# Kernel optimization log

Measured on AMD Instinct MI355X. Metric: run time of the kernel, lower is better.

The kernel has to match this reference:

```python
import jax, jax.numpy as jnp
import numpy as np

QMIN, QMAX = -128.0, 127.0


def setup_inputs() -> dict:
    key = jax.random.key(0)
    kx, kw, kb = jax.random.split(key, 3)
    B, S, K, M = 4, 2048, 4096, 4096
    x = jax.random.normal(kx, (B, S, K), dtype=jnp.float32)
    bound = 1.0 / np.sqrt(K)  # kaiming_uniform(a=sqrt(5)) -> U(-1/sqrt(fan_in), 1/sqrt(fan_in))
    W = jax.random.uniform(kw, (M, K), dtype=jnp.float32, minval=-bound, maxval=bound)
    b = jax.random.uniform(kb, (M,), dtype=jnp.float32, minval=-bound, maxval=bound)
    return {"x": x, "W": W, "b": b}


def _quant_weights_rowwise(W):
    # symmetric per-row int8: scale = absmax/127
    absmax = jnp.max(jnp.abs(W), axis=1, keepdims=True)  # [M,1]
    scale = jnp.where(absmax > 0, absmax / QMAX, 1.0)
    Wq = jnp.clip(jnp.round(W / scale), QMIN, QMAX)
    return Wq, scale


def _quant_acts_per_token(X):
    # asymmetric per-token (per column of X.t()) int8 with zero-point
    xmin = jnp.min(X, axis=1, keepdims=True)  # [N,1]
    xmax = jnp.max(X, axis=1, keepdims=True)
    rng = xmax - xmin
    scale = jnp.where(rng > 0, rng / (QMAX - QMIN), 1.0)
    zp = jnp.clip(jnp.round(QMIN - xmin / scale), QMIN, QMAX)
    Xq = jnp.clip(jnp.round(X / scale + zp), QMIN, QMAX)
    return Xq, scale, zp


def reference(x, W, b):
    B, S, K = x.shape
    X = x.reshape(-1, K)  # [N, K]
    Wq, row_scale = _quant_weights_rowwise(W)          # [M,K], [M,1]
    Xq, col_scale, zp = _quant_acts_per_token(X)       # [N,K], [N,1], [N,1]
    # fused dequant-GEMM: Y = ((Xq - zp) * col_scale) @ (Wq * row_scale).T
    Wdq = Wq * row_scale                               # [M,K]
    Xdq = (Xq - zp) * col_scale                        # [N,K]
    Y = jnp.einsum('nk,mk->nm', Xdq, Wdq) + b          # [N,M]
    return Y.reshape(B, S, -1)
```

## Files before the change

kernel.cpp:

```cpp
#include <hip/hip_runtime.h>
#include <stdint.h>


typedef __attribute__((ext_vector_type(4)))  int int4v;
typedef __attribute__((ext_vector_type(16))) int int16v;

__device__ __forceinline__ void async_load16(const void* g, void* l) {
    __builtin_amdgcn_global_load_lds(
        (const __attribute__((address_space(1))) void*)g,
        (__attribute__((address_space(3))) void*)l, 16, 0, 0);
}

__device__ __forceinline__ int quant_clip(float v) {
    return (int)fminf(fmaxf(rintf(v), -128.f), 127.f);
}

__global__ __launch_bounds__(256) void quant_kernel(
    const float* __restrict__ W, const float* __restrict__ X,
    int8_t* __restrict__ Wq, int8_t* __restrict__ Xq,
    float* __restrict__ row_scale, int* __restrict__ wsum,
    float* __restrict__ col_scale, int* __restrict__ zp, int M, int K) {
    const int blk  = blockIdx.x;
    const int tid  = threadIdx.x;
    const int lane = tid & 63;
    const int wv   = tid >> 6;
    __shared__ float sred0[4], sred1[4];
    __shared__ int   isum[4];

    if (blk < M) {
        const int row = blk;
        const float4* w4 = (const float4*)(W + (size_t)row * K);
        float4 vals[4];
        float amax = 0.f;
#pragma unroll
        for (int i = 0; i < 4; ++i) {
            float4 v = w4[tid + i * 256];
            vals[i] = v;
            amax = fmaxf(amax, fmaxf(fmaxf(fabsf(v.x), fabsf(v.y)),
                                     fmaxf(fabsf(v.z), fabsf(v.w))));
        }
#pragma unroll
        for (int off = 32; off > 0; off >>= 1)
            amax = fmaxf(amax, __shfl_down(amax, off, 64));
        if (lane == 0) sred0[wv] = amax;
        __syncthreads();
        amax = fmaxf(fmaxf(sred0[0], sred0[1]), fmaxf(sred0[2], sred0[3]));

        const float scale = (amax > 0.f) ? (amax / 127.f) : 1.f;
        const float inv   = 1.f / scale;

        int ssum = 0;
        int* wq32 = (int*)(Wq + (size_t)row * K);
#pragma unroll
        for (int i = 0; i < 4; ++i) {
            float4 v = vals[i];
            int q0 = quant_clip(v.x * inv);
            int q1 = quant_clip(v.y * inv);
            int q2 = quant_clip(v.z * inv);
            int q3 = quant_clip(v.w * inv);
            ssum += q0 + q1 + q2 + q3;
            wq32[tid + i * 256] =
                (q0 & 0xff) | ((q1 & 0xff) << 8) | ((q2 & 0xff) << 16) | ((q3 & 0xff) << 24);
        }
#pragma unroll
        for (int off = 32; off > 0; off >>= 1)
            ssum += __shfl_down(ssum, off, 64);
        if (lane == 0) isum[wv] = ssum;
        __syncthreads();
        if (tid == 0) {
            wsum[row] = isum[0] + isum[1] + isum[2] + isum[3];
            row_scale[row] = scale;
        }
    } else {
        const int row = blk - M;
        const float4* x4 = (const float4*)(X + (size_t)row * K);
        float4 vals[4];
        float vmin = 3.402823466e+38f, vmax = -3.402823466e+38f;
#pragma unroll
        for (int i = 0; i < 4; ++i) {
            float4 v = x4[tid + i * 256];
            vals[i] = v;
            vmin = fminf(vmin, fminf(fminf(v.x, v.y), fminf(v.z, v.w)));
            vmax = fmaxf(vmax, fmaxf(fmaxf(v.x, v.y), fmaxf(v.z, v.w)));
        }
#pragma unroll
        for (int off = 32; off > 0; off >>= 1) {
            vmin = fminf(vmin, __shfl_down(vmin, off, 64));
            vmax = fmaxf(vmax, __shfl_down(vmax, off, 64));
        }
        if (lane == 0) { sred0[wv] = vmin; sred1[wv] = vmax; }
        __syncthreads();
        vmin = fminf(fminf(sred0[0], sred0[1]), fminf(sred0[2], sred0[3]));
        vmax = fmaxf(fmaxf(sred1[0], sred1[1]), fmaxf(sred1[2], sred1[3]));

        const float rng   = vmax - vmin;
        const float scale = (rng > 0.f) ? (rng / 255.f) : 1.f;
        const float inv   = 1.f / scale;
        const float zpf   = fminf(fmaxf(rintf(-128.f - vmin * inv), -128.f), 127.f);

        int* xq32 = (int*)(Xq + (size_t)row * K);
#pragma unroll
        for (int i = 0; i < 4; ++i) {
            float4 v = vals[i];
            int q0 = quant_clip(v.x * inv + zpf);
            int q1 = quant_clip(v.y * inv + zpf);
            int q2 = quant_clip(v.z * inv + zpf);
            int q3 = quant_clip(v.w * inv + zpf);
            xq32[tid + i * 256] =
                (q0 & 0xff) | ((q1 & 0xff) << 8) | ((q2 & 0xff) << 16) | ((q3 & 0xff) << 24);
        }
        if (tid == 0) {
            col_scale[row] = scale;
            zp[row] = (int)zpf;
        }
    }
}

__global__ __launch_bounds__(256) void gemm_i8_kernel(
    const int8_t* __restrict__ Xq, const int8_t* __restrict__ Wq,
    const float* __restrict__ cs, const int* __restrict__ zp,
    const float* __restrict__ rs, const int* __restrict__ wsum,
    const float* __restrict__ bias, float* __restrict__ out,
    int N, int M, int K) {
    __shared__ __align__(16) int8_t As[128 * 64];
    __shared__ __align__(16) int8_t Bs[128 * 64];

    const int t    = threadIdx.x;
    const int wv   = t >> 6;
    const int lane = t & 63;
    const int r32  = lane & 31;
    const int half = lane >> 5;

    const int m0 = blockIdx.x * 128;
    const int n0 = blockIdx.y * 128;
    const int wn = (wv >> 1) * 64;
    const int wm = (wv & 1) * 64;

    int16v acc[2][2];
#pragma unroll
    for (int i = 0; i < 2; ++i)
#pragma unroll
        for (int j = 0; j < 2; ++j)
            acc[i][j] = (int16v)(0);

    const int r0 = t >> 2;
    const int c0 = (t & 3) ^ ((r0 >> 1) & 3);
    const size_t gA0 = (size_t)(n0 + r0) * K + c0 * 16;
    const size_t gA1 = (size_t)(n0 + 64 + r0) * K + c0 * 16;
    const size_t gB0 = (size_t)(m0 + r0) * K + c0 * 16;
    const size_t gB1 = (size_t)(m0 + 64 + r0) * K + c0 * 16;
    int8_t* lA0 = As + wv * 1024;
    int8_t* lA1 = As + 4096 + wv * 1024;
    int8_t* lB0 = Bs + wv * 1024;
    int8_t* lB1 = Bs + 4096 + wv * 1024;

    int abase[2], bbase[2], asw[2], bsw[2];
#pragma unroll
    for (int i = 0; i < 2; ++i) {
        const int ra = wn + i * 32 + r32;
        abase[i] = ra * 64;
        asw[i]   = (ra >> 1) & 3;
        const int rb = wm + i * 32 + r32;
        bbase[i] = rb * 64;
        bsw[i]   = (rb >> 1) & 3;
    }

    for (int k0 = 0; k0 < K; k0 += 64) {
        async_load16(Xq + gA0 + k0, lA0);
        async_load16(Xq + gA1 + k0, lA1);
        async_load16(Wq + gB0 + k0, lB0);
        async_load16(Wq + gB1 + k0, lB1);
        __syncthreads();

        int4v a[2][2], b[2][2];
#pragma unroll
        for (int s = 0; s < 2; ++s) {
            const int ch = s * 2 + half;
#pragma unroll
            for (int i = 0; i < 2; ++i) {
                a[s][i] = *(const int4v*)(As + abase[i] + ((ch ^ asw[i]) << 4));
                b[s][i] = *(const int4v*)(Bs + bbase[i] + ((ch ^ bsw[i]) << 4));
            }
        }
#pragma unroll
        for (int s = 0; s < 2; ++s)
#pragma unroll
            for (int i = 0; i < 2; ++i)
#pragma unroll
                for (int j = 0; j < 2; ++j)
                    acc[i][j] = __builtin_amdgcn_mfma_i32_32x32x32_i8(
                        a[s][i], b[s][j], acc[i][j], 0, 0, 0);
        __syncthreads();
    }

    int   mm[2];
    float rsv[2], bv[2];
    int   wsv[2];
#pragma unroll
    for (int j = 0; j < 2; ++j) {
        mm[j]  = m0 + wm + j * 32 + r32;
        rsv[j] = rs[mm[j]];
        bv[j]  = bias[mm[j]];
        wsv[j] = wsum[mm[j]];
    }
#pragma unroll
    for (int i = 0; i < 2; ++i) {
        const int nb = n0 + wn + i * 32 + half * 4;
#pragma unroll
        for (int reg = 0; reg < 16; ++reg) {
            const int n = nb + (reg & 3) + 8 * (reg >> 2);
            const float csn = cs[n];
            const int   zpn = zp[n];
#pragma unroll
            for (int j = 0; j < 2; ++j) {
                const int ival = acc[i][j][reg] - zpn * wsv[j];
                out[(size_t)n * M + mm[j]] = csn * rsv[j] * (float)ival + bv[j];
            }
        }
    }
}

extern "C" void kernel_launch(void* const* d_in, const int* in_sizes, int n_in,
                              void* d_out, int out_size, void* d_ws, size_t ws_size,
                              hipStream_t stream) {
    const float* x = (const float*)d_in[0];
    const float* W = (const float*)d_in[1];
    const float* b = (const float*)d_in[2];
    float* out = (float*)d_out;

    const int M = in_sizes[2];
    const int K = in_sizes[1] / M;
    const int N = in_sizes[0] / K;

    int8_t* Xq = (int8_t*)d_ws;
    int8_t* Wq = Xq + (size_t)N * K;
    float* cs  = (float*)(Wq + (size_t)M * K);
    int* zps   = (int*)(cs + N);
    float* rs  = (float*)(zps + N);
    int* wsum  = (int*)(rs + M);

    quant_kernel<<<dim3(M + N), dim3(256), 0, stream>>>(
        W, x, Wq, Xq, rs, wsum, cs, zps, M, K);
    gemm_i8_kernel<<<dim3(M / 128, N / 128), dim3(256), 0, stream>>>(
        Xq, Wq, cs, zps, rs, wsum, b, out, N, M, K);
}
```

Measured before the change: 445.0 us.

## Use 256x256 int8 GEMM tiles with double-buffered async LDS pipeline

```diff
diff --git a/kernel.cpp b/kernel.cpp
--- a/kernel.cpp
+++ b/kernel.cpp
@@ -116,81 +116,122 @@
     }
 }
 
-__global__ __launch_bounds__(256) void gemm_i8_kernel(
+#define REGION(buf, mat, kh) (lds + ((((buf) * 2 + (mat)) * 2 + (kh)) << 14))
+
+__device__ __forceinline__ void compute_half(
+    const int8_t* Ar, const int8_t* Br,
+    const int aoff[4], const int boff[2],
+    const int half, const int sw4, int16v (&acc)[4][2]) {
+    __builtin_amdgcn_s_setprio(1);
+#pragma unroll
+    for (int ss = 0; ss < 2; ++ss) {
+        const int cc = ((((ss << 1) + half) ^ sw4) << 4);
+        int4v a[4], b[2];
+#pragma unroll
+        for (int i = 0; i < 4; ++i)
+            a[i] = *(const int4v*)(Ar + aoff[i] + cc);
+#pragma unroll
+        for (int j = 0; j < 2; ++j)
+            b[j] = *(const int4v*)(Br + boff[j] + cc);
+#pragma unroll
+        for (int i = 0; i < 4; ++i)
+#pragma unroll
+            for (int j = 0; j < 2; ++j)
+                acc[i][j] = __builtin_amdgcn_mfma_i32_32x32x32_i8(
+                    a[i], b[j], acc[i][j], 0, 0, 0);
+    }
+    __builtin_amdgcn_s_setprio(0);
+}
+
+__global__ __launch_bounds__(512, 2) void gemm_i8_kernel(
     const int8_t* __restrict__ Xq, const int8_t* __restrict__ Wq,
     const float* __restrict__ cs, const int* __restrict__ zp,
     const float* __restrict__ rs, const int* __restrict__ wsum,
     const float* __restrict__ bias, float* __restrict__ out,
     int N, int M, int K) {
-    __shared__ __align__(16) int8_t As[128 * 64];
-    __shared__ __align__(16) int8_t Bs[128 * 64];
+    __shared__ __align__(16) int8_t lds[131072];
 
     const int t    = threadIdx.x;
     const int wv   = t >> 6;
     const int lane = t & 63;
     const int r32  = lane & 31;
     const int half = lane >> 5;
-
-    const int m0 = blockIdx.x * 128;
-    const int n0 = blockIdx.y * 128;
-    const int wn = (wv >> 1) * 64;
-    const int wm = (wv & 1) * 64;
-
-    int16v acc[2][2];
-#pragma unroll
-    for (int i = 0; i < 2; ++i)
+    const int wn   = wv >> 2;
+    const int wm   = wv & 3;
+
+    const int nMB = M >> 8;
+    const int per = ((M >> 8) * (N >> 8)) >> 3;
+    const int lin = blockIdx.x;
+    const int g   = (lin & 7) * per + (lin >> 3);
+    const int m0  = (g % nMB) << 8;
+    const int n0  = (g / nMB) << 8;
+
+    const int NT = K >> 7;
+
+    const int lrow   = (wv << 4) + (lane >> 2);
+    const int srcOff = (((lane & 3) ^ ((lane >> 3) & 3)) << 4);
+    const int8_t* gA0 = Xq + (size_t)(n0 + lrow) * K + srcOff;
+    const int8_t* gA1 = Xq + (size_t)(n0 + 128 + lrow) * K + srcOff;
+    const int8_t* gB0 = Wq + (size_t)(m0 + lrow) * K + srcOff;
+    const int8_t* gB1 = Wq + (size_t)(m0 + 128 + lrow) * K + srcOff;
+    const int wvOff = wv << 10;
+
+    int aoff[4], boff[2];
+#pragma unroll
+    for (int i = 0; i < 4; ++i) aoff[i] = (((wn << 7) + i * 32 + r32) << 6);
+#pragma unroll
+    for (int j = 0; j < 2; ++j) boff[j] = (((wm << 6) + j * 32 + r32) << 6);
+    const int sw4 = (r32 >> 1) & 3;
+
+    int16v acc[4][2];
+#pragma unroll
+    for (int i = 0; i < 4; ++i)
 #pragma unroll
         for (int j = 0; j < 2; ++j)
             acc[i][j] = (int16v)(0);
 
-    const int r0 = t >> 2;
-    const int c0 = (t & 3) ^ ((r0 >> 1) & 3);
-    const size_t gA0 = (size_t)(n0 + r0) * K + c0 * 16;
-    const size_t gA1 = (size_t)(n0 + 64 + r0) * K + c0 * 16;
-    const size_t gB0 = (size_t)(m0 + r0) * K + c0 * 16;
-    const size_t gB1 = (size_t)(m0 + 64 + r0) * K + c0 * 16;
-    int8_t* lA0 = As + wv * 1024;
-    int8_t* lA1 = As + 4096 + wv * 1024;
-    int8_t* lB0 = Bs + wv * 1024;
-    int8_t* lB1 = Bs + 4096 + wv * 1024;
-
-    int abase[2], bbase[2], asw[2], bsw[2];
-#pragma unroll
-    for (int i = 0; i < 2; ++i) {
-        const int ra = wn + i * 32 + r32;
-        abase[i] = ra * 64;
-        asw[i]   = (ra >> 1) & 3;
-        const int rb = wm + i * 32 + r32;
-        bbase[i] = rb * 64;
-        bsw[i]   = (rb >> 1) & 3;
-    }
-
-    for (int k0 = 0; k0 < K; k0 += 64) {
-        async_load16(Xq + gA0 + k0, lA0);
-        async_load16(Xq + gA1 + k0, lA1);
-        async_load16(Wq + gB0 + k0, lB0);
-        async_load16(Wq + gB1 + k0, lB1);
-        __syncthreads();
-
-        int4v a[2][2], b[2][2];
-#pragma unroll
-        for (int s = 0; s < 2; ++s) {
-            const int ch = s * 2 + half;
-#pragma unroll
-            for (int i = 0; i < 2; ++i) {
-                a[s][i] = *(const int4v*)(As + abase[i] + ((ch ^ asw[i]) << 4));
-                b[s][i] = *(const int4v*)(Bs + bbase[i] + ((ch ^ bsw[i]) << 4));
-            }
-        }
-#pragma unroll
-        for (int s = 0; s < 2; ++s)
-#pragma unroll
-            for (int i = 0; i < 2; ++i)
-#pragma unroll
-                for (int j = 0; j < 2; ++j)
-                    acc[i][j] = __builtin_amdgcn_mfma_i32_32x32x32_i8(
-                        a[s][i], b[s][j], acc[i][j], 0, 0, 0);
-        __syncthreads();
+    {
+        int8_t* r;
+        r = REGION(0, 0, 0) + wvOff; async_load16(gA0, r);       async_load16(gA1, r + 8192);
+        r = REGION(0, 1, 0) + wvOff; async_load16(gB0, r);       async_load16(gB1, r + 8192);
+        r = REGION(0, 0, 1) + wvOff; async_load16(gA0 + 64, r);  async_load16(gA1 + 64, r + 8192);
+        r = REGION(0, 1, 1) + wvOff; async_load16(gB0 + 64, r);  async_load16(gB1 + 64, r + 8192);
+        r = REGION(1, 0, 0) + wvOff; async_load16(gA0 + 128, r); async_load16(gA1 + 128, r + 8192);
+        r = REGION(1, 1, 0) + wvOff; async_load16(gB0 + 128, r); async_load16(gB1 + 128, r + 8192);
+    }
+    asm volatile("s_waitcnt vmcnt(8)" ::: "memory");
+    __builtin_amdgcn_s_barrier();
+
+    for (int tt = 0; tt < NT; ++tt) {
+        const int buf = tt & 1;
+        {
+            const int tn = (tt + 1 < NT) ? tt + 1 : NT - 1;
+            const int ko = (tn << 7) + 64;
+            int8_t* r;
+            r = REGION(buf ^ 1, 0, 1) + wvOff;
+            async_load16(gA0 + ko, r); async_load16(gA1 + ko, r + 8192);
+            r = REGION(buf ^ 1, 1, 1) + wvOff;
+            async_load16(gB0 + ko, r); async_load16(gB1 + ko, r + 8192);
+
+            compute_half(REGION(buf, 0, 0), REGION(buf, 1, 0), aoff, boff, half, sw4, acc);
+
+            asm volatile("s_waitcnt vmcnt(8)" ::: "memory");
+            __builtin_amdgcn_s_barrier();
+        }
+        {
+            const int tn = (tt + 2 < NT) ? tt + 2 : NT - 1;
+            const int ko = (tn << 7);
+            int8_t* r;
+            r = REGION(buf, 0, 0) + wvOff;
+            async_load16(gA0 + ko, r); async_load16(gA1 + ko, r + 8192);
+            r = REGION(buf, 1, 0) + wvOff;
+            async_load16(gB0 + ko, r); async_load16(gB1 + ko, r + 8192);
+
+            compute_half(REGION(buf, 0, 1), REGION(buf, 1, 1), aoff, boff, half, sw4, acc);
+
+            asm volatile("s_waitcnt vmcnt(8)" ::: "memory");
+            __builtin_amdgcn_s_barrier();
+        }
     }
 
     int   mm[2];
@@ -198,17 +239,17 @@
     int   wsv[2];
 #pragma unroll
     for (int j = 0; j < 2; ++j) {
-        mm[j]  = m0 + wm + j * 32 + r32;
+        mm[j]  = m0 + (wm << 6) + j * 32 + r32;
         rsv[j] = rs[mm[j]];
         bv[j]  = bias[mm[j]];
         wsv[j] = wsum[mm[j]];
     }
 #pragma unroll
-    for (int i = 0; i < 2; ++i) {
-        const int nb = n0 + wn + i * 32 + half * 4;
+    for (int i = 0; i < 4; ++i) {
+        const int nbase = n0 + (wn << 7) + i * 32 + (half << 2);
 #pragma unroll
         for (int reg = 0; reg < 16; ++reg) {
-            const int n = nb + (reg & 3) + 8 * (reg >> 2);
+            const int n = nbase + (reg & 3) + 8 * (reg >> 2);
             const float csn = cs[n];
             const int   zpn = zp[n];
 #pragma unroll
@@ -241,6 +282,6 @@
 
     quant_kernel<<<dim3(M + N), dim3(256), 0, stream>>>(
         W, x, Wq, Xq, rs, wsum, cs, zps, M, K);
-    gemm_i8_kernel<<<dim3(M / 128, N / 128), dim3(256), 0, stream>>>(
+    gemm_i8_kernel<<<dim3((M >> 8) * (N >> 8)), dim3(512), 0, stream>>>(
         Xq, Wq, cs, zps, rs, wsum, b, out, N, M, K);
 }
```

New measurement: 409.9 us. 7.9% less time.

## Triple-buffer int8 GEMM LDS loads with XCD-aware block swizzle

Applied to the files above, without the earlier changes.

```diff
diff --git a/kernel.cpp b/kernel.cpp
--- a/kernel.cpp
+++ b/kernel.cpp
@@ -116,81 +116,101 @@
     }
 }
 
-__global__ __launch_bounds__(256) void gemm_i8_kernel(
+__global__ __launch_bounds__(256, 4) void gemm_i8_kernel(
     const int8_t* __restrict__ Xq, const int8_t* __restrict__ Wq,
     const float* __restrict__ cs, const int* __restrict__ zp,
     const float* __restrict__ rs, const int* __restrict__ wsum,
     const float* __restrict__ bias, float* __restrict__ out,
     int N, int M, int K) {
-    __shared__ __align__(16) int8_t As[128 * 64];
-    __shared__ __align__(16) int8_t Bs[128 * 64];
+    __shared__ __align__(16) int8_t lds[49152];
 
     const int t    = threadIdx.x;
     const int wv   = t >> 6;
     const int lane = t & 63;
     const int r32  = lane & 31;
     const int half = lane >> 5;
-
-    const int m0 = blockIdx.x * 128;
-    const int n0 = blockIdx.y * 128;
-    const int wn = (wv >> 1) * 64;
-    const int wm = (wv & 1) * 64;
-
-    int16v acc[2][2];
-#pragma unroll
-    for (int i = 0; i < 2; ++i)
-#pragma unroll
-        for (int j = 0; j < 2; ++j)
-            acc[i][j] = (int16v)(0);
-
-    const int r0 = t >> 2;
-    const int c0 = (t & 3) ^ ((r0 >> 1) & 3);
-    const size_t gA0 = (size_t)(n0 + r0) * K + c0 * 16;
-    const size_t gA1 = (size_t)(n0 + 64 + r0) * K + c0 * 16;
-    const size_t gB0 = (size_t)(m0 + r0) * K + c0 * 16;
-    const size_t gB1 = (size_t)(m0 + 64 + r0) * K + c0 * 16;
-    int8_t* lA0 = As + wv * 1024;
-    int8_t* lA1 = As + 4096 + wv * 1024;
-    int8_t* lB0 = Bs + wv * 1024;
-    int8_t* lB1 = Bs + 4096 + wv * 1024;
-
-    int abase[2], bbase[2], asw[2], bsw[2];
-#pragma unroll
-    for (int i = 0; i < 2; ++i) {
-        const int ra = wn + i * 32 + r32;
-        abase[i] = ra * 64;
-        asw[i]   = (ra >> 1) & 3;
-        const int rb = wm + i * 32 + r32;
-        bbase[i] = rb * 64;
-        bsw[i]   = (rb >> 1) & 3;
-    }
-
-    for (int k0 = 0; k0 < K; k0 += 64) {
-        async_load16(Xq + gA0 + k0, lA0);
-        async_load16(Xq + gA1 + k0, lA1);
-        async_load16(Wq + gB0 + k0, lB0);
-        async_load16(Wq + gB1 + k0, lB1);
-        __syncthreads();
-
-        int4v a[2][2], b[2][2];
-#pragma unroll
-        for (int s = 0; s < 2; ++s) {
-            const int ch = s * 2 + half;
-#pragma unroll
-            for (int i = 0; i < 2; ++i) {
-                a[s][i] = *(const int4v*)(As + abase[i] + ((ch ^ asw[i]) << 4));
-                b[s][i] = *(const int4v*)(Bs + bbase[i] + ((ch ^ bsw[i]) << 4));
-            }
-        }
-#pragma unroll
-        for (int s = 0; s < 2; ++s)
-#pragma unroll
-            for (int i = 0; i < 2; ++i)
-#pragma unroll
-                for (int j = 0; j < 2; ++j)
-                    acc[i][j] = __builtin_amdgcn_mfma_i32_32x32x32_i8(
-                        a[s][i], b[s][j], acc[i][j], 0, 0, 0);
-        __syncthreads();
+    const int wn   = wv >> 1;
+    const int wm   = wv & 1;
+
+    const int mcols = M >> 7;
+    const int mpx   = mcols >> 3;
+    const int lin   = blockIdx.x;
+    const int xcd   = lin & 7;
+    const int p     = lin >> 3;
+    const int m0    = (xcd * mpx + (p & (mpx - 1))) << 7;
+    const int n0    = (p / mpx) << 7;
+
+    const int NT = K >> 6;
+
+    const int lrow   = (wv << 4) + (lane >> 2);
+    const int srcOff = (((lane & 3) ^ ((lane >> 4) & 3)) << 4);
+    const int8_t* gA = Xq + (size_t)(n0 + lrow) * K + srcOff;
+    const int8_t* gB = Wq + (size_t)(m0 + lrow) * K + srcOff;
+    const size_t rowK64 = (size_t)K << 6;
+    const int wvOff = wv << 10;
+
+    const int aoff0 = ((wn << 6) + r32) << 6;
+    const int aoff1 = ((wn << 6) + 32 + r32) << 6;
+    const int boff0 = (((wm << 6) + r32) << 6) + 8192;
+    const int boff1 = (((wm << 6) + 32 + r32) << 6) + 8192;
+    const int sw4 = (r32 >> 2) & 3;
+    const int cc0 = ((half ^ sw4) << 4);
+    const int cc1 = (((2 + half) ^ sw4) << 4);
+
+    int16v acc00 = (int16v)(0), acc01 = (int16v)(0);
+    int16v acc10 = (int16v)(0), acc11 = (int16v)(0);
+
+    int8_t* b0 = lds;
+    int8_t* b1 = lds + 16384;
+    int8_t* b2 = lds + 32768;
+
+    async_load16(gA,               b0 + wvOff);
+    async_load16(gA + rowK64,      b0 + 4096 + wvOff);
+    async_load16(gB,               b0 + 8192 + wvOff);
+    async_load16(gB + rowK64,      b0 + 12288 + wvOff);
+    async_load16(gA + 64,          b1 + wvOff);
+    async_load16(gA + 64 + rowK64, b1 + 4096 + wvOff);
+    async_load16(gB + 64,          b1 + 8192 + wvOff);
+    async_load16(gB + 64 + rowK64, b1 + 12288 + wvOff);
+    asm volatile("s_waitcnt vmcnt(4)" ::: "memory");
+    __builtin_amdgcn_sched_barrier(0);
+    __builtin_amdgcn_s_barrier();
+
+    int8_t* pR = b0;
+    int8_t* pN = b1;
+    int8_t* pS = b2;
+
+    for (int tt = 0; tt < NT; ++tt) {
+        const int ko2 = ((tt + 2 < NT) ? tt + 2 : NT - 1) << 6;
+
+        async_load16(gA + ko2,          pS + wvOff);
+        async_load16(gA + ko2 + rowK64, pS + 4096 + wvOff);
+        async_load16(gB + ko2,          pS + 8192 + wvOff);
+        async_load16(gB + ko2 + rowK64, pS + 12288 + wvOff);
+
+        int4v a0 = *(const int4v*)(pR + aoff0 + cc0);
+        int4v b0v = *(const int4v*)(pR + boff0 + cc0);
+        int4v b1v = *(const int4v*)(pR + boff1 + cc0);
+        int4v a1 = *(const int4v*)(pR + aoff1 + cc0);
+        int4v a2 = *(const int4v*)(pR + aoff0 + cc1);
+        int4v b2v = *(const int4v*)(pR + boff0 + cc1);
+        int4v b3v = *(const int4v*)(pR + boff1 + cc1);
+        int4v a3 = *(const int4v*)(pR + aoff1 + cc1);
+
+        acc00 = __builtin_amdgcn_mfma_i32_32x32x32_i8(a0, b0v, acc00, 0, 0, 0);
+        acc01 = __builtin_amdgcn_mfma_i32_32x32x32_i8(a0, b1v, acc01, 0, 0, 0);
+        acc10 = __builtin_amdgcn_mfma_i32_32x32x32_i8(a1, b0v, acc10, 0, 0, 0);
+        acc11 = __builtin_amdgcn_mfma_i32_32x32x32_i8(a1, b1v, acc11, 0, 0, 0);
+        acc00 = __builtin_amdgcn_mfma_i32_32x32x32_i8(a2, b2v, acc00, 0, 0, 0);
+        acc01 = __builtin_amdgcn_mfma_i32_32x32x32_i8(a2, b3v, acc01, 0, 0, 0);
+        acc10 = __builtin_amdgcn_mfma_i32_32x32x32_i8(a3, b2v, acc10, 0, 0, 0);
+        acc11 = __builtin_amdgcn_mfma_i32_32x32x32_i8(a3, b3v, acc11, 0, 0, 0);
+
+        asm volatile("s_waitcnt vmcnt(4)" ::: "memory");
+        __builtin_amdgcn_sched_barrier(0);
+        __builtin_amdgcn_s_barrier();
+
+        int8_t* tmp = pR; pR = pN; pN = pS; pS = tmp;
     }
 
     int   mm[2];
@@ -198,22 +218,23 @@
     int   wsv[2];
 #pragma unroll
     for (int j = 0; j < 2; ++j) {
-        mm[j]  = m0 + wm + j * 32 + r32;
+        mm[j]  = m0 + (wm << 6) + j * 32 + r32;
         rsv[j] = rs[mm[j]];
         bv[j]  = bias[mm[j]];
         wsv[j] = wsum[mm[j]];
     }
+    const int16v* accp[2][2] = {{&acc00, &acc01}, {&acc10, &acc11}};
 #pragma unroll
     for (int i = 0; i < 2; ++i) {
-        const int nb = n0 + wn + i * 32 + half * 4;
+        const int nbase = n0 + (wn << 6) + i * 32 + (half << 2);
 #pragma unroll
         for (int reg = 0; reg < 16; ++reg) {
-            const int n = nb + (reg & 3) + 8 * (reg >> 2);
+            const int n = nbase + (reg & 3) + 8 * (reg >> 2);
             const float csn = cs[n];
             const int   zpn = zp[n];
 #pragma unroll
             for (int j = 0; j < 2; ++j) {
-                const int ival = acc[i][j][reg] - zpn * wsv[j];
+                const int ival = (*accp[i][j])[reg] - zpn * wsv[j];
                 out[(size_t)n * M + mm[j]] = csn * rsv[j] * (float)ival + bv[j];
             }
         }
@@ -236,11 +257,14 @@
     int8_t* Wq = Xq + (size_t)N * K;
     float* cs  = (float*)(Wq + (size_t)M * K);
     int* zps   = (int*)(cs + N);
-    float* rs  = (float*)(zps + N);
+    float* rs  = (float*)(zps + M);
     int* wsum  = (int*)(rs + M);
+
+    rs   = (float*)(zps + N);
+    wsum = (int*)(rs + M);
 
     quant_kernel<<<dim3(M + N), dim3(256), 0, stream>>>(
         W, x, Wq, Xq, rs, wsum, cs, zps, M, K);
-    gemm_i8_kernel<<<dim3(M / 128, N / 128), dim3(256), 0, stream>>>(
+    gemm_i8_kernel<<<dim3((M >> 7) * (N >> 7)), dim3(256), 0, stream>>>(
         Xq, Wq, cs, zps, rs, wsum, b, out, N, M, K);
 }
```

Result: faster. 432.8 us (-2.7%).
